# Kernel optimization log

Measured on AMD Instinct MI355X. Metric: run time of the kernel, lower is better.

## Reference

```python
import jax, jax.numpy as jnp
from jax import lax
import numpy as np

B, T, IN, H = 512, 2048, 6, 32


def _gru_dir(x, Wih, bih, Whh, bhh, reverse):
    # x: [B, T, in]; PyTorch GRU gate order: r, z, n
    xp = jnp.einsum('bti,gi->btg', x, Wih) + bih  # [B, T, 3H] precompute input GEMM
    h0 = jnp.zeros((x.shape[0], Whh.shape[1]), x.dtype)

    def step(h, xt):
        gh = h @ Whh.T + bhh                      # [B, 3H]
        xr, xz, xn = jnp.split(xt, 3, axis=-1)
        hr, hz, hn = jnp.split(gh, 3, axis=-1)
        r = jax.nn.sigmoid(xr + hr)
        z = jax.nn.sigmoid(xz + hz)
        n = jnp.tanh(xn + r * hn)
        h_new = (1.0 - z) * n + z * h
        return h_new, h_new

    xs = jnp.swapaxes(xp, 0, 1)                   # [T, B, 3H]
    _, hs = lax.scan(step, h0, xs, reverse=reverse)  # ys aligned to time index
    return jnp.swapaxes(hs, 0, 1)                 # [B, T, H]


def setup_inputs() -> dict:
    key = jax.random.key(0)
    ks = jax.random.split(key, 32)
    s = 1.0 / np.sqrt(H)
    u = lambda k, shp: jax.random.uniform(k, shp, jnp.float32, -s, s)
    inp = {'x': jax.random.normal(ks[0], (B, T, IN), jnp.float32)}
    i = 1
    for l, din in ((0, IN), (1, 2 * H)):
        for d in ('f', 'b'):
            inp[f'Wih_l{l}_{d}'] = u(ks[i], (3 * H, din)); i += 1
            inp[f'Whh_l{l}_{d}'] = u(ks[i], (3 * H, H)); i += 1
            inp[f'bih_l{l}_{d}'] = u(ks[i], (3 * H,)); i += 1
            inp[f'bhh_l{l}_{d}'] = u(ks[i], (3 * H,)); i += 1
    inp['fc1_w'] = u(ks[i], (16, 2 * H)); i += 1
    inp['fc1_b'] = u(ks[i], (16,)); i += 1
    inp['fc2_w'] = u(ks[i], (1, 16)); i += 1
    inp['fc2_b'] = u(ks[i], (1,))
    return inp


def reference(x, Wih_l0_f, Whh_l0_f, bih_l0_f, bhh_l0_f,
              Wih_l0_b, Whh_l0_b, bih_l0_b, bhh_l0_b,
              Wih_l1_f, Whh_l1_f, bih_l1_f, bhh_l1_f,
              Wih_l1_b, Whh_l1_b, bih_l1_b, bhh_l1_b,
              fc1_w, fc1_b, fc2_w, fc2_b):
    # layer 0 bidirectional
    f0 = _gru_dir(x, Wih_l0_f, bih_l0_f, Whh_l0_f, bhh_l0_f, reverse=False)
    b0 = _gru_dir(x, Wih_l0_b, bih_l0_b, Whh_l0_b, bhh_l0_b, reverse=True)
    h0 = jnp.concatenate([f0, b0], axis=-1)       # [B, T, 2H]; inter-layer dropout: eval mode -> identity
    # layer 1 bidirectional
    f1 = _gru_dir(h0, Wih_l1_f, bih_l1_f, Whh_l1_f, bhh_l1_f, reverse=False)
    b1 = _gru_dir(h0, Wih_l1_b, bih_l1_b, Whh_l1_b, bhh_l1_b, reverse=True)
    out = jnp.concatenate([f1, b1], axis=-1)      # [B, T, 2H]
    pooled = jnp.mean(out, axis=1)                # [B, 2H]
    h = jax.nn.relu(pooled @ fc1_w.T + fc1_b)     # dropout: eval mode -> identity
    return h @ fc2_w.T + fc2_b                    # [B, 1]
```

## Files before the change

kernel.cpp:

```cpp
#include <hip/hip_runtime.h>

#define TB  512
#define TT  2048
#define HID 32

typedef _Float16 f16;
typedef float f32x2 __attribute__((ext_vector_type(2)));


#define PKFMA(ACC, A, B) \
  asm("v_pk_fma_f32 %0, %1, %2, %0" : "+v"(ACC) : "v"(A), "v"(B))

#define TWO_LOG2E 2.88539008177792682f

__device__ __forceinline__ float half_swap(float x, int half){
#if __has_builtin(__builtin_amdgcn_permlane32_swap)
  typedef unsigned uv2 __attribute__((ext_vector_type(2)));
  uv2 r = __builtin_amdgcn_permlane32_swap(__float_as_uint(x), __float_as_uint(x),
                                           false, false);
  return __uint_as_float(half ? r.x : r.y);
#else
  (void)half;
  return __shfl_xor(x, 32, 64);
#endif
}

__global__ __launch_bounds__(64,1)
void gru_l0(const float* __restrict__ x,
            const float* __restrict__ Wih_f, const float* __restrict__ Whh_f,
            const float* __restrict__ bih_f, const float* __restrict__ bhh_f,
            const float* __restrict__ Wih_b, const float* __restrict__ Whh_b,
            const float* __restrict__ bih_b, const float* __restrict__ bhh_b,
            f16* __restrict__ h0)
{
  const int job  = blockIdx.x;
  const int b    = job >> 1;
  const int dir  = job & 1;
  const int lane = threadIdx.x;
  const int j    = lane & 31;
  const int half = lane >> 5;

  const float* Wih = dir ? Wih_b : Wih_f;
  const float* Whh = dir ? Whh_b : Whh_f;
  const float* bih = dir ? bih_b : bih_f;
  const float* bhh = dir ? bhh_b : bhh_f;

  const int mrow = half * 32 + j;
  const int nrow = 64 + j;

  f32x2 wh_m2[16], wh_n2[16];
  f32x2 wi_m2[3],  wi_n2[3];
  {
    const float4* wm4 = (const float4*)(Whh + mrow*32);
#pragma unroll
    for (int q=0;q<8;q++){ float4 v=wm4[q];
      wh_m2[2*q]   = f32x2{v.x, v.y};
      wh_m2[2*q+1] = f32x2{v.z, v.w}; }
    const float4* wn4 = (const float4*)(Whh + nrow*32);
#pragma unroll
    for (int q=0;q<8;q++){ float4 v=wn4[q];
      wh_n2[2*q]   = f32x2{v.x, v.y};
      wh_n2[2*q+1] = f32x2{v.z, v.w}; }
#pragma unroll
    for (int i=0;i<3;i++){
      wi_m2[i] = f32x2{Wih[mrow*6+2*i], Wih[mrow*6+2*i+1]};
      wi_n2[i] = f32x2{Wih[nrow*6+2*i], Wih[nrow*6+2*i+1]};
    }
  }
  const float b_m   = bih[mrow] + bhh[mrow];
  const float b_ihn = bih[nrow];
  const float b_hhn = bhh[nrow];

  __shared__ __align__(16) float hlds[32];

  double hj = 0.;
  float  hjf = 0.f;

  const long t0    = dir ? (TT-1) : 0;
  const long tstep = dir ? -1 : 1;
  const float* xrow = x + ((size_t)b*TT + t0)*6;
  const long  xinc = tstep*6;
  f16* hout = h0 + ((size_t)b*TT + t0)*64 + dir*32;
  const long hinc = tstep*64;

  f32x2 hp[16];
#pragma unroll
  for (int k=0;k<16;k++) hp[k]=f32x2{0.f,0.f};

#define L0_STEP(XV)                                                          \
  {                                                                          \
    f32x2 SX2 = f32x2{0.f,0.f}, SN2 = f32x2{0.f,0.f};                        \
    PKFMA(SX2, wi_m2[0], XV[0]); PKFMA(SN2, wi_n2[0], XV[0]);                \
    PKFMA(SX2, wi_m2[1], XV[1]); PKFMA(SN2, wi_n2[1], XV[1]);                \
    PKFMA(SX2, wi_m2[2], XV[2]); PKFMA(SN2, wi_n2[2], XV[2]);                \
    float sx  = SX2.x + SX2.y;                                               \
    float sxn = SN2.x + SN2.y;                                               \
    f32x2 A0=f32x2{0.f,0.f}, A1=f32x2{0.f,0.f};                              \
    f32x2 A2=f32x2{0.f,0.f}, A3=f32x2{0.f,0.f};                              \
    f32x2 C0=f32x2{0.f,0.f}, C1=f32x2{0.f,0.f};                              \
    f32x2 C2=f32x2{0.f,0.f}, C3=f32x2{0.f,0.f};                              \
    _Pragma("unroll")                                                        \
    for (int k=0;k<4;k++){                                                   \
      PKFMA(A0, wh_m2[4*k],   hp[4*k]);                                      \
      PKFMA(A1, wh_m2[4*k+1], hp[4*k+1]);                                    \
      PKFMA(A2, wh_m2[4*k+2], hp[4*k+2]);                                    \
      PKFMA(A3, wh_m2[4*k+3], hp[4*k+3]);                                    \
      PKFMA(C0, wh_n2[4*k],   hp[4*k]);                                      \
      PKFMA(C1, wh_n2[4*k+1], hp[4*k+1]);                                    \
      PKFMA(C2, wh_n2[4*k+2], hp[4*k+2]);                                    \
      PKFMA(C3, wh_n2[4*k+3], hp[4*k+3]);                                    \
    }                                                                        \
    f32x2 At = A0+A1+A2+A3;                                                  \
    f32x2 Ct = C0+C1+C2+C3;                                                  \
    float hm   = At.x + At.y;                                                \
    float sn_h = Ct.x + Ct.y;                                                \
    float vf   = hm + sx + b_m;                                              \
    float varg = half ? -vf : vf;                                            \
    float ef   = __builtin_amdgcn_exp2f(varg * -1.44269504088896341f);       \
    float gmf  = __builtin_amdgcn_rcpf(1.f + ef);                            \
    float wf   = half_swap(gmf, half);                                       \
    float c1 = (sxn + b_ihn) * TWO_LOG2E;                                    \
    float c2 = (sn_h + b_hhn) * TWO_LOG2E;                                   \
    float e2 = __builtin_amdgcn_exp2f(fmaf(gmf, c2, c1));                    \
    float nnf= 1.f - 2.f*__builtin_amdgcn_rcpf(1.f + e2);                    \
    float hnf = fmaf(wf, nnf - hjf, hjf);                                    \
    if (lane < 32){ hlds[j] = hnf; hout[j] = (f16)hnf; }                     \
    hout += hinc;                                                            \
    hj = fma((double)wf, (double)nnf - hj, hj);                              \
    hjf = (float)hj;                                                         \
    {                                                                        \
      const float4* h4 = (const float4*)hlds;                                \
      _Pragma("unroll")                                                      \
      for (int q=0;q<8;q++){ float4 v=h4[q];                                 \
        hp[2*q]   = f32x2{v.x, v.y};                                         \
        hp[2*q+1] = f32x2{v.z, v.w}; }                                       \
    }                                                                        \
  }

  f32x2 xa[3], xb[3];
  {
    const float2* p=(const float2*)xrow;
    xa[0]=f32x2{p[0].x,p[0].y}; xa[1]=f32x2{p[1].x,p[1].y}; xa[2]=f32x2{p[2].x,p[2].y};
    const float2* q=(const float2*)(xrow + xinc);
    xb[0]=f32x2{q[0].x,q[0].y}; xb[1]=f32x2{q[1].x,q[1].y}; xb[2]=f32x2{q[2].x,q[2].y};
  }
  const float* xld = xrow + 2*xinc;

#pragma unroll 1
  for (int it=0; it<TT; it+=2){
    L0_STEP(xa)
    if (it+2 < TT){
      const float2* p=(const float2*)xld;
      xa[0]=f32x2{p[0].x,p[0].y}; xa[1]=f32x2{p[1].x,p[1].y}; xa[2]=f32x2{p[2].x,p[2].y};
      xld += xinc;
    }
    L0_STEP(xb)
    if (it+3 < TT){
      const float2* p=(const float2*)xld;
      xb[0]=f32x2{p[0].x,p[0].y}; xb[1]=f32x2{p[1].x,p[1].y}; xb[2]=f32x2{p[2].x,p[2].y};
      xld += xinc;
    }
  }
#undef L0_STEP
}

__global__ __launch_bounds__(128,2)
void gru_l1(const f16* __restrict__ h0,
            const float* __restrict__ Wih_f, const float* __restrict__ Whh_f,
            const float* __restrict__ bih_f, const float* __restrict__ bhh_f,
            const float* __restrict__ Wih_b, const float* __restrict__ Whh_b,
            const float* __restrict__ bih_b, const float* __restrict__ bhh_b,
            float* __restrict__ pooled)
{
  const int job  = blockIdx.x;
  const int b    = job >> 1;
  const int dir  = job & 1;
  const int tid  = threadIdx.x;
  const int wid  = tid >> 6;
  const int lane = tid & 63;
  const int j    = lane & 31;
  const int half = lane >> 5;

  const float* Wih = dir ? Wih_b : Wih_f;
  const float* Whh = dir ? Whh_b : Whh_f;
  const float* bih = dir ? bih_b : bih_f;
  const float* bhh = dir ? bhh_b : bhh_f;

  const int mrow = half * 32 + j;
  const int nrow = 64 + j;

  __shared__ __align__(16) float hlds[32];
  __shared__ __align__(16) float ring[16*64];
  __shared__ __align__(16) float fx[16][64];
  __shared__ __align__(16) float fn[16][64];

  const f16* h0b = h0 + (size_t)b*TT*64;
#define ROWF(LT) (h0b + (size_t)(dir ? (TT-1-(LT)) : (LT))*64)

  f32x2 wreg[48];
  float b_m=0.f, b_ihn=0.f, b_hhn=0.f;

  if (wid == 1){
    const float4* wr4 = (const float4*)(Wih + (size_t)j*64      + half*32);
    const float4* wz4 = (const float4*)(Wih + (size_t)(32+j)*64 + half*32);
    const float4* wn4 = (const float4*)(Wih + (size_t)(64+j)*64 + half*32);
#pragma unroll
    for (int q=0;q<8;q++){ float4 v=wr4[q];
      wreg[2*q]   = f32x2{v.x,v.y};
      wreg[2*q+1] = f32x2{v.z,v.w}; }
#pragma unroll
    for (int q=0;q<8;q++){ float4 v=wz4[q];
      wreg[16+2*q]   = f32x2{v.x,v.y};
      wreg[16+2*q+1] = f32x2{v.z,v.w}; }
#pragma unroll
    for (int q=0;q<8;q++){ float4 v=wn4[q];
      wreg[32+2*q]   = f32x2{v.x,v.y};
      wreg[32+2*q+1] = f32x2{v.z,v.w}; }
  } else {
    const float4* hm4 = (const float4*)(Whh + mrow*32);
#pragma unroll
    for (int q=0;q<8;q++){ float4 v=hm4[q];
      wreg[2*q]   = f32x2{v.x,v.y};
      wreg[2*q+1] = f32x2{v.z,v.w}; }
    const float4* hn4 = (const float4*)(Whh + nrow*32);
#pragma unroll
    for (int q=0;q<8;q++){ float4 v=hn4[q];
      wreg[16+2*q]   = f32x2{v.x,v.y};
      wreg[16+2*q+1] = f32x2{v.z,v.w}; }
    b_m   = bih[mrow] + bhh[mrow];
    b_ihn = bih[nrow];
    b_hhn = bhh[nrow];
    if (lane < 32) hlds[lane] = 0.f;
  }

#define PRODUCE(S)                                                           \
  {                                                                          \
    const int slot = (S)&15;                                                 \
    const float4* s4 = (const float4*)(ring + slot*64 + half*32);            \
    f32x2 R0=f32x2{0.f,0.f}, R1=f32x2{0.f,0.f};                              \
    f32x2 Z0=f32x2{0.f,0.f}, Z1=f32x2{0.f,0.f};                              \
    f32x2 N0=f32x2{0.f,0.f}, N1=f32x2{0.f,0.f};                              \
    _Pragma("unroll")                                                        \
    for (int q=0;q<8;q++){ float4 v=s4[q];                                   \
      f32x2 lo = f32x2{v.x,v.y}, hi = f32x2{v.z,v.w};                        \
      PKFMA(R0, wreg[2*q],      lo);                                         \
      PKFMA(R1, wreg[2*q+1],    hi);                                         \
      PKFMA(Z0, wreg[16+2*q],   lo);                                         \
      PKFMA(Z1, wreg[16+2*q+1], hi);                                         \
      PKFMA(N0, wreg[32+2*q],   lo);                                         \
      PKFMA(N1, wreg[32+2*q+1], hi);                                         \
    }                                                                        \
    f32x2 Rt = R0+R1; f32x2 Zt = Z0+Z1; f32x2 Nt = N0+N1;                    \
    float rP = Rt.x+Rt.y, zP = Zt.x+Zt.y, nP = Nt.x+Nt.y;                    \
    float rF = rP + half_swap(rP, half);                                     \
    float zF = zP + half_swap(zP, half);                                     \
    fx[slot][lane] = half ? zF : rF;                                         \
    fn[slot][lane] = nP + half_swap(nP, half);                               \
  }

#define CORE(SX, SN)                                                         \
  {                                                                          \
    f32x2 A0=f32x2{0.f,0.f}, A1=f32x2{0.f,0.f};                              \
    f32x2 A2=f32x2{0.f,0.f}, A3=f32x2{0.f,0.f};                              \
    f32x2 C0=f32x2{0.f,0.f}, C1=f32x2{0.f,0.f};                              \
    f32x2 C2=f32x2{0.f,0.f}, C3=f32x2{0.f,0.f};                              \
    {                                                                        \
      const float4* h4 = (const float4*)hlds;                                \
      _Pragma("unroll")                                                      \
      for (int q=0;q<4;q++){                                                 \
        float4 v0=h4[2*q], v1=h4[2*q+1];                                     \
        f32x2 l0 = f32x2{v0.x,v0.y}, h0_ = f32x2{v0.z,v0.w};                 \
        f32x2 l1 = f32x2{v1.x,v1.y}, h1_ = f32x2{v1.z,v1.w};                 \
        PKFMA(A0, wreg[4*q],      l0);                                       \
        PKFMA(A1, wreg[4*q+1],    h0_);                                      \
        PKFMA(A2, wreg[4*q+2],    l1);                                       \
        PKFMA(A3, wreg[4*q+3],    h1_);                                      \
        PKFMA(C0, wreg[16+4*q],   l0);                                       \
        PKFMA(C1, wreg[16+4*q+1], h0_);                                      \
        PKFMA(C2, wreg[16+4*q+2], l1);                                       \
        PKFMA(C3, wreg[16+4*q+3], h1_);                                      \
      }                                                                      \
    }                                                                        \
    f32x2 At = A0+A1+A2+A3;                                                  \
    f32x2 Ct = C0+C1+C2+C3;                                                  \
    float hm   = At.x + At.y;                                                \
    float sn_h = Ct.x + Ct.y;                                                \
    float vf   = hm + (SX) + b_m;                                            \
    float varg = half ? -vf : vf;                                            \
    float ef   = __builtin_amdgcn_exp2f(varg * -1.44269504088896341f);       \
    float gmf  = __builtin_amdgcn_rcpf(1.f + ef);                            \
    float wf   = half_swap(gmf, half);                                       \
    float c1 = ((SN) + b_ihn) * TWO_LOG2E;                                   \
    float c2 = (sn_h + b_hhn) * TWO_LOG2E;                                   \
    float e2 = __builtin_amdgcn_exp2f(fmaf(gmf, c2, c1));                    \
    float nnf= 1.f - 2.f*__builtin_amdgcn_rcpf(1.f + e2);                    \
    float hnf = fmaf(wf, nnf - hjf, hjf);                                    \
    if (lane < 32) hlds[j] = hnf;                                            \
    hj = fma((double)wf, (double)nnf - hj, hj);                              \
    hjf = (float)hj;                                                         \
    psum += hj;                                                              \
  }

  double hj = 0., psum = 0.;
  float  hjf = 0.f;
  float pr[8];

  if (wid == 1){
    float pr0[16];
#pragma unroll
    for (int k=0;k<16;k++){
      int lt = k; if (lt > TT-1) lt = TT-1;
      pr0[k] = (float)ROWF(lt)[lane];
    }
#pragma unroll
    for (int k=0;k<16;k++) ring[k*64 + lane] = pr0[k];
#pragma unroll
    for (int k=0;k<8;k++){
      int lt = 16+k; if (lt > TT-1) lt = TT-1;
      pr[k] = (float)ROWF(lt)[lane];
    }
    PRODUCE(0) PRODUCE(1) PRODUCE(2) PRODUCE(3)
    PRODUCE(4) PRODUCE(5) PRODUCE(6) PRODUCE(7)
  }

#pragma unroll 1
  for (int t=0; t<TT; t+=8){
    __syncthreads();
    if (wid == 0){
      float sxa[8], sna[8];
#pragma unroll
      for (int k=0;k<8;k++){
        sxa[k] = fx[(t+k)&15][lane];
        sna[k] = fn[(t+k)&15][lane];
      }
      CORE(sxa[0], sna[0]) CORE(sxa[1], sna[1])
      CORE(sxa[2], sna[2]) CORE(sxa[3], sna[3])
      CORE(sxa[4], sna[4]) CORE(sxa[5], sna[5])
      CORE(sxa[6], sna[6]) CORE(sxa[7], sna[7])
    } else {
#pragma unroll
      for (int k=0;k<8;k++) ring[((t+16+k)&15)*64 + lane] = pr[k];
#pragma unroll
      for (int k=0;k<8;k++){
        int lt = t+24+k; if (lt > TT-1) lt = TT-1;
        pr[k] = (float)ROWF(lt)[lane];
      }
      if (t+8 <= TT-1){
        PRODUCE(t+8)
        PRODUCE(t+9) PRODUCE(t+10) PRODUCE(t+11)
        PRODUCE(t+12) PRODUCE(t+13) PRODUCE(t+14) PRODUCE(t+15)
      }
    }
  }
#undef PRODUCE
#undef CORE
#undef ROWF

  if (wid == 0 && lane < 32)
    pooled[(size_t)b*64 + dir*32 + j] = (float)psum;
}

__global__ void fc_ep(const float* __restrict__ pooled,
                      const float* __restrict__ fc1w, const float* __restrict__ fc1b,
                      const float* __restrict__ fc2w, const float* __restrict__ fc2b,
                      float* __restrict__ out)
{
  int b = blockIdx.x*blockDim.x + threadIdx.x;
  if (b >= TB) return;
  float v[64];
  const float4* p4 = (const float4*)(pooled + (size_t)b*64);
#pragma unroll
  for (int q=0;q<16;q++){ float4 t=p4[q];
    v[4*q]  =t.x*(1.f/TT); v[4*q+1]=t.y*(1.f/TT);
    v[4*q+2]=t.z*(1.f/TT); v[4*q+3]=t.w*(1.f/TT); }
  float acc = fc2b[0];
#pragma unroll
  for (int g=0; g<16; g++){
    float s = fc1b[g];
    const float4* w4 = (const float4*)(fc1w + g*64);
#pragma unroll
    for (int q=0;q<16;q++){ float4 w=w4[q];
      s=fmaf(w.x,v[4*q],s);   s=fmaf(w.y,v[4*q+1],s);
      s=fmaf(w.z,v[4*q+2],s); s=fmaf(w.w,v[4*q+3],s); }
    s = fmaxf(s, 0.f);
    acc = fmaf(fc2w[g], s, acc);
  }
  out[b] = acc;
}

extern "C" void kernel_launch(void* const* d_in, const int* in_sizes, int n_in,
                              void* d_out, int out_size, void* d_ws, size_t ws_size,
                              hipStream_t stream)
{
  (void)in_sizes; (void)n_in; (void)out_size;

  const float* x     = (const float*)d_in[0];
  const float* Wih0f = (const float*)d_in[1];
  const float* Whh0f = (const float*)d_in[2];
  const float* bih0f = (const float*)d_in[3];
  const float* bhh0f = (const float*)d_in[4];
  const float* Wih0b = (const float*)d_in[5];
  const float* Whh0b = (const float*)d_in[6];
  const float* bih0b = (const float*)d_in[7];
  const float* bhh0b = (const float*)d_in[8];
  const float* Wih1f = (const float*)d_in[9];
  const float* Whh1f = (const float*)d_in[10];
  const float* bih1f = (const float*)d_in[11];
  const float* bhh1f = (const float*)d_in[12];
  const float* Wih1b = (const float*)d_in[13];
  const float* Whh1b = (const float*)d_in[14];
  const float* bih1b = (const float*)d_in[15];
  const float* bhh1b = (const float*)d_in[16];
  const float* fc1w  = (const float*)d_in[17];
  const float* fc1b  = (const float*)d_in[18];
  const float* fc2w  = (const float*)d_in[19];
  const float* fc2b  = (const float*)d_in[20];

  const size_t POOLED_BYTES = (size_t)TB * 64 * sizeof(float);
  const size_t PER_B        = (size_t)TT * 64 * sizeof(f16);
  float* pooled = (float*)d_ws;
  f16*   h0     = (f16*)((char*)d_ws + POOLED_BYTES);

  size_t avail = (ws_size > POOLED_BYTES) ? (ws_size - POOLED_BYTES) : 0;
  int Bc = (int)(avail / PER_B);
  if (Bc < 1)  Bc = 1;
  if (Bc > TB) Bc = TB;
  int nch = (TB + Bc - 1) / Bc;
  int Bce = (TB + nch - 1) / nch;

  for (int b0 = 0; b0 < TB; b0 += Bce) {
    int bc = (TB - b0 < Bce) ? (TB - b0) : Bce;
    hipLaunchKernelGGL(gru_l0, dim3(2*bc), dim3(64), 0, stream,
                       x + (size_t)b0*TT*6,
                       Wih0f,Whh0f,bih0f,bhh0f, Wih0b,Whh0b,bih0b,bhh0b, h0);
    hipLaunchKernelGGL(gru_l1, dim3(2*bc), dim3(128), 0, stream,
                       h0,
                       Wih1f,Whh1f,bih1f,bhh1f, Wih1b,Whh1b,bih1b,bhh1b,
                       pooled + (size_t)b0*64);
  }
  hipLaunchKernelGGL(fc_ep, dim3(2), dim3(256), 0, stream,
                     pooled, fc1w, fc1b, fc2w, fc2b, (float*)d_out);
}
```

Before: 1.765 ms.

## Split recurrent matvec over K halves with cross-half reduction in both GRU layers

Previously each lane owned one full 32-long row: lanes 0-31 computed the r gate, lanes 32-63 the z gate, and every lane also computed the n row, so the n matvec was duplicated across halves. Now each half of the wave computes partial dot products over 16 of the 32 hidden inputs for all three gates, and the halves are combined with a permlane32 swap. This cuts per-lane FMAs on the serial critical path from 32 to 24 packed ops and halves the LDS reads of h per step. In exchange it adds three cross-half swaps per step, and every lane now evaluates both sigmoids redundantly.

```diff
diff --git a/kernel.cpp b/kernel.cpp
--- a/kernel.cpp
+++ b/kernel.cpp
@@ -11,6 +11,7 @@
 #define PKFMA(ACC, A, B) \
   asm("v_pk_fma_f32 %0, %1, %2, %0" : "+v"(ACC) : "v"(A), "v"(B))
 
+#define LOG2E     1.44269504088896341f
 #define TWO_LOG2E 2.88539008177792682f
 
 __device__ __forceinline__ float half_swap(float x, int half){
@@ -24,6 +25,19 @@
   return __shfl_xor(x, 32, 64);
 #endif
 }
+
+#define GATE_TAIL(HM_R, HM_Z, SN_H, XR, XZ, XNF)                             \
+    float vr = (HM_R) + (XR) + b_r;                                          \
+    float vz = (HM_Z) + (XZ) + b_z;                                          \
+    float er = __builtin_amdgcn_exp2f(vr * -LOG2E);                          \
+    float ez = __builtin_amdgcn_exp2f(vz *  LOG2E);                          \
+    float gr = __builtin_amdgcn_rcpf(1.f + er);                  \
+    float wf = __builtin_amdgcn_rcpf(1.f + ez);                 \
+    float c1 = ((XNF) + b_ihn) * TWO_LOG2E;                                  \
+    float c2 = ((SN_H) + b_hhn) * TWO_LOG2E;                                 \
+    float e2 = __builtin_amdgcn_exp2f(fmaf(gr, c2, c1));                     \
+    float nnf= 1.f - 2.f*__builtin_amdgcn_rcpf(1.f + e2);                    \
+    float hnf = fmaf(wf, nnf - hjf, hjf);
 
 __global__ __launch_bounds__(64,1)
 void gru_l0(const float* __restrict__ x,
@@ -45,31 +59,32 @@
   const float* bih = dir ? bih_b : bih_f;
   const float* bhh = dir ? bhh_b : bhh_f;
 
-  const int mrow = half * 32 + j;
-  const int nrow = 64 + j;
-
-  f32x2 wh_m2[16], wh_n2[16];
-  f32x2 wi_m2[3],  wi_n2[3];
+  f32x2 wr2[8], wz2[8], wn2[8];
+  f32x2 xwr[3], xwz[3], xwn[3];
   {
-    const float4* wm4 = (const float4*)(Whh + mrow*32);
-#pragma unroll
-    for (int q=0;q<8;q++){ float4 v=wm4[q];
-      wh_m2[2*q]   = f32x2{v.x, v.y};
-      wh_m2[2*q+1] = f32x2{v.z, v.w}; }
-    const float4* wn4 = (const float4*)(Whh + nrow*32);
-#pragma unroll
-    for (int q=0;q<8;q++){ float4 v=wn4[q];
-      wh_n2[2*q]   = f32x2{v.x, v.y};
-      wh_n2[2*q+1] = f32x2{v.z, v.w}; }
+    const float4* r4 = (const float4*)(Whh + (size_t)j*32      + half*16);
+    const float4* z4 = (const float4*)(Whh + (size_t)(32+j)*32 + half*16);
+    const float4* n4 = (const float4*)(Whh + (size_t)(64+j)*32 + half*16);
+#pragma unroll
+    for (int q=0;q<4;q++){ float4 v=r4[q];
+      wr2[2*q]=f32x2{v.x,v.y}; wr2[2*q+1]=f32x2{v.z,v.w}; }
+#pragma unroll
+    for (int q=0;q<4;q++){ float4 v=z4[q];
+      wz2[2*q]=f32x2{v.x,v.y}; wz2[2*q+1]=f32x2{v.z,v.w}; }
+#pragma unroll
+    for (int q=0;q<4;q++){ float4 v=n4[q];
+      wn2[2*q]=f32x2{v.x,v.y}; wn2[2*q+1]=f32x2{v.z,v.w}; }
 #pragma unroll
     for (int i=0;i<3;i++){
-      wi_m2[i] = f32x2{Wih[mrow*6+2*i], Wih[mrow*6+2*i+1]};
-      wi_n2[i] = f32x2{Wih[nrow*6+2*i], Wih[nrow*6+2*i+1]};
-    }
-  }
-  const float b_m   = bih[mrow] + bhh[mrow];
-  const float b_ihn = bih[nrow];
-  const float b_hhn = bhh[nrow];
+      xwr[i] = f32x2{Wih[(size_t)j*6+2*i],      Wih[(size_t)j*6+2*i+1]};
+      xwz[i] = f32x2{Wih[(size_t)(32+j)*6+2*i], Wih[(size_t)(32+j)*6+2*i+1]};
+      xwn[i] = f32x2{Wih[(size_t)(64+j)*6+2*i], Wih[(size_t)(64+j)*6+2*i+1]};
+    }
+  }
+  const float b_r   = bih[j]    + bhh[j];
+  const float b_z   = bih[32+j] + bhh[32+j];
+  const float b_ihn = bih[64+j];
+  const float b_hhn = bhh[64+j];
 
   __shared__ __align__(16) float hlds[32];
 
@@ -83,55 +98,43 @@
   f16* hout = h0 + ((size_t)b*TT + t0)*64 + dir*32;
   const long hinc = tstep*64;
 
-  f32x2 hp[16];
-#pragma unroll
-  for (int k=0;k<16;k++) hp[k]=f32x2{0.f,0.f};
+  f32x2 hp[8];
+#pragma unroll
+  for (int k=0;k<8;k++) hp[k]=f32x2{0.f,0.f};
 
 #define L0_STEP(XV)                                                          \
   {                                                                          \
-    f32x2 SX2 = f32x2{0.f,0.f}, SN2 = f32x2{0.f,0.f};                        \
-    PKFMA(SX2, wi_m2[0], XV[0]); PKFMA(SN2, wi_n2[0], XV[0]);                \
-    PKFMA(SX2, wi_m2[1], XV[1]); PKFMA(SN2, wi_n2[1], XV[1]);                \
-    PKFMA(SX2, wi_m2[2], XV[2]); PKFMA(SN2, wi_n2[2], XV[2]);                \
-    float sx  = SX2.x + SX2.y;                                               \
-    float sxn = SN2.x + SN2.y;                                               \
-    f32x2 A0=f32x2{0.f,0.f}, A1=f32x2{0.f,0.f};                              \
-    f32x2 A2=f32x2{0.f,0.f}, A3=f32x2{0.f,0.f};                              \
-    f32x2 C0=f32x2{0.f,0.f}, C1=f32x2{0.f,0.f};                              \
-    f32x2 C2=f32x2{0.f,0.f}, C3=f32x2{0.f,0.f};                              \
+    f32x2 XR2=f32x2{0.f,0.f}, XZ2=f32x2{0.f,0.f}, XN2=f32x2{0.f,0.f};        \
+    PKFMA(XR2, xwr[0], XV[0]); PKFMA(XZ2, xwz[0], XV[0]); PKFMA(XN2, xwn[0], XV[0]); \
+    PKFMA(XR2, xwr[1], XV[1]); PKFMA(XZ2, xwz[1], XV[1]); PKFMA(XN2, xwn[1], XV[1]); \
+    PKFMA(XR2, xwr[2], XV[2]); PKFMA(XZ2, xwz[2], XV[2]); PKFMA(XN2, xwn[2], XV[2]); \
+    float xr = XR2.x+XR2.y, xz = XZ2.x+XZ2.y, xnf = XN2.x+XN2.y;             \
+    f32x2 R0=f32x2{0.f,0.f}, R1=f32x2{0.f,0.f};                              \
+    f32x2 Z0=f32x2{0.f,0.f}, Z1=f32x2{0.f,0.f};                              \
+    f32x2 N0=f32x2{0.f,0.f}, N1=f32x2{0.f,0.f};                              \
     _Pragma("unroll")                                                        \
     for (int k=0;k<4;k++){                                                   \
-      PKFMA(A0, wh_m2[4*k],   hp[4*k]);                                      \
-      PKFMA(A1, wh_m2[4*k+1], hp[4*k+1]);                                    \
-      PKFMA(A2, wh_m2[4*k+2], hp[4*k+2]);                                    \
-      PKFMA(A3, wh_m2[4*k+3], hp[4*k+3]);                                    \
-      PKFMA(C0, wh_n2[4*k],   hp[4*k]);                                      \
-      PKFMA(C1, wh_n2[4*k+1], hp[4*k+1]);                                    \
-      PKFMA(C2, wh_n2[4*k+2], hp[4*k+2]);                                    \
-      PKFMA(C3, wh_n2[4*k+3], hp[4*k+3]);                                    \
+      PKFMA(R0, wr2[2*k],   hp[2*k]);                                        \
+      PKFMA(R1, wr2[2*k+1], hp[2*k+1]);                                      \
+      PKFMA(Z0, wz2[2*k],   hp[2*k]);                                        \
+      PKFMA(Z1, wz2[2*k+1], hp[2*k+1]);                                      \
+      PKFMA(N0, wn2[2*k],   hp[2*k]);                                        \
+      PKFMA(N1, wn2[2*k+1], hp[2*k+1]);                                      \
     }                                                                        \
-    f32x2 At = A0+A1+A2+A3;                                                  \
-    f32x2 Ct = C0+C1+C2+C3;                                                  \
-    float hm   = At.x + At.y;                                                \
-    float sn_h = Ct.x + Ct.y;                                                \
-    float vf   = hm + sx + b_m;                                              \
-    float varg = half ? -vf : vf;                                            \
-    float ef   = __builtin_amdgcn_exp2f(varg * -1.44269504088896341f);       \
-    float gmf  = __builtin_amdgcn_rcpf(1.f + ef);                            \
-    float wf   = half_swap(gmf, half);                                       \
-    float c1 = (sxn + b_ihn) * TWO_LOG2E;                                    \
-    float c2 = (sn_h + b_hhn) * TWO_LOG2E;                                   \
-    float e2 = __builtin_amdgcn_exp2f(fmaf(gmf, c2, c1));                    \
-    float nnf= 1.f - 2.f*__builtin_amdgcn_rcpf(1.f + e2);                    \
-    float hnf = fmaf(wf, nnf - hjf, hjf);                                    \
+    f32x2 Rt=R0+R1; f32x2 Zt=Z0+Z1; f32x2 Nt=N0+N1;                          \
+    float rP = Rt.x+Rt.y, zP = Zt.x+Zt.y, nP = Nt.x+Nt.y;                    \
+    float hm_r = rP + half_swap(rP, half);                                   \
+    float hm_z = zP + half_swap(zP, half);                                   \
+    float sn_h = nP + half_swap(nP, half);                                   \
+    GATE_TAIL(hm_r, hm_z, sn_h, xr, xz, xnf)                                 \
     if (lane < 32){ hlds[j] = hnf; hout[j] = (f16)hnf; }                     \
     hout += hinc;                                                            \
     hj = fma((double)wf, (double)nnf - hj, hj);                              \
     hjf = (float)hj;                                                         \
     {                                                                        \
-      const float4* h4 = (const float4*)hlds;                                \
+      const float4* h4 = (const float4*)(hlds + half*16);                    \
       _Pragma("unroll")                                                      \
-      for (int q=0;q<8;q++){ float4 v=h4[q];                                 \
+      for (int q=0;q<4;q++){ float4 v=h4[q];                                 \
         hp[2*q]   = f32x2{v.x, v.y};                                         \
         hp[2*q+1] = f32x2{v.z, v.w}; }                                       \
     }                                                                        \
@@ -186,19 +189,16 @@
   const float* bih = dir ? bih_b : bih_f;
   const float* bhh = dir ? bhh_b : bhh_f;
 
-  const int mrow = half * 32 + j;
-  const int nrow = 64 + j;
-
-  __shared__ __align__(16) float hlds[32];
-  __shared__ __align__(16) float ring[16*64];
-  __shared__ __align__(16) float fx[16][64];
-  __shared__ __align__(16) float fn[16][64];
+  __shared__ __align__(16) float  hlds[32];
+  __shared__ __align__(16) float  ring[16*64];
+  __shared__ __align__(16) float2 fxz[16][64];
+  __shared__ __align__(16) float  fnn[16][64];
 
   const f16* h0b = h0 + (size_t)b*TT*64;
 #define ROWF(LT) (h0b + (size_t)(dir ? (TT-1-(LT)) : (LT))*64)
 
   f32x2 wreg[48];
-  float b_m=0.f, b_ihn=0.f, b_hhn=0.f;
+  float b_r=0.f, b_z=0.f, b_ihn=0.f, b_hhn=0.f;
 
   if (wid == 1){
     const float4* wr4 = (const float4*)(Wih + (size_t)j*64      + half*32);
@@ -217,19 +217,22 @@
       wreg[32+2*q]   = f32x2{v.x,v.y};
       wreg[32+2*q+1] = f32x2{v.z,v.w}; }
   } else {
-    const float4* hm4 = (const float4*)(Whh + mrow*32);
-#pragma unroll
-    for (int q=0;q<8;q++){ float4 v=hm4[q];
-      wreg[2*q]   = f32x2{v.x,v.y};
-      wreg[2*q+1] = f32x2{v.z,v.w}; }
-    const float4* hn4 = (const float4*)(Whh + nrow*32);
-#pragma unroll
-    for (int q=0;q<8;q++){ float4 v=hn4[q];
-      wreg[16+2*q]   = f32x2{v.x,v.y};
-      wreg[16+2*q+1] = f32x2{v.z,v.w}; }
-    b_m   = bih[mrow] + bhh[mrow];
-    b_ihn = bih[nrow];
-    b_hhn = bhh[nrow];
+    const float4* r4 = (const float4*)(Whh + (size_t)j*32      + half*16);
+    const float4* z4 = (const float4*)(Whh + (size_t)(32+j)*32 + half*16);
+    const float4* n4 = (const float4*)(Whh + (size_t)(64+j)*32 + half*16);
+#pragma unroll
+    for (int q=0;q<4;q++){ float4 v=r4[q];
+      wreg[2*q]=f32x2{v.x,v.y}; wreg[2*q+1]=f32x2{v.z,v.w}; }
+#pragma unroll
+    for (int q=0;q<4;q++){ float4 v=z4[q];
+      wreg[8+2*q]=f32x2{v.x,v.y}; wreg[8+2*q+1]=f32x2{v.z,v.w}; }
+#pragma unroll
+    for (int q=0;q<4;q++){ float4 v=n4[q];
+      wreg[16+2*q]=f32x2{v.x,v.y}; wreg[16+2*q+1]=f32x2{v.z,v.w}; }
+    b_r   = bih[j]    + bhh[j];
+    b_z   = bih[32+j] + bhh[32+j];
+    b_ihn = bih[64+j];
+    b_hhn = bhh[64+j];
     if (lane < 32) hlds[lane] = 0.f;
   }
 
@@ -254,47 +257,34 @@
     float rP = Rt.x+Rt.y, zP = Zt.x+Zt.y, nP = Nt.x+Nt.y;                    \
     float rF = rP + half_swap(rP, half);                                     \
     float zF = zP + half_swap(zP, half);                                     \
-    fx[slot][lane] = half ? zF : rF;                                         \
-    fn[slot][lane] = nP + half_swap(nP, half);                               \
-  }
-
-#define CORE(SX, SN)                                                         \
+    fxz[slot][lane] = float2{rF, zF};                                        \
+    fnn[slot][lane] = nP + half_swap(nP, half);                              \
+  }
+
+#define CORE(FXZ, FN)                                                        \
   {                                                                          \
-    f32x2 A0=f32x2{0.f,0.f}, A1=f32x2{0.f,0.f};                              \
-    f32x2 A2=f32x2{0.f,0.f}, A3=f32x2{0.f,0.f};                              \
-    f32x2 C0=f32x2{0.f,0.f}, C1=f32x2{0.f,0.f};                              \
-    f32x2 C2=f32x2{0.f,0.f}, C3=f32x2{0.f,0.f};                              \
+    f32x2 R0=f32x2{0.f,0.f}, R1=f32x2{0.f,0.f};                              \
+    f32x2 Z0=f32x2{0.f,0.f}, Z1=f32x2{0.f,0.f};                              \
+    f32x2 N0=f32x2{0.f,0.f}, N1=f32x2{0.f,0.f};                              \
     {                                                                        \
-      const float4* h4 = (const float4*)hlds;                                \
+      const float4* h4 = (const float4*)(hlds + half*16);                    \
       _Pragma("unroll")                                                      \
-      for (int q=0;q<4;q++){                                                 \
-        float4 v0=h4[2*q], v1=h4[2*q+1];                                     \
-        f32x2 l0 = f32x2{v0.x,v0.y}, h0_ = f32x2{v0.z,v0.w};                 \
-        f32x2 l1 = f32x2{v1.x,v1.y}, h1_ = f32x2{v1.z,v1.w};                 \
-        PKFMA(A0, wreg[4*q],      l0);                                       \
-        PKFMA(A1, wreg[4*q+1],    h0_);                                      \
-        PKFMA(A2, wreg[4*q+2],    l1);                                       \
-        PKFMA(A3, wreg[4*q+3],    h1_);                                      \
-        PKFMA(C0, wreg[16+4*q],   l0);                                       \
-        PKFMA(C1, wreg[16+4*q+1], h0_);                                      \
-        PKFMA(C2, wreg[16+4*q+2], l1);                                       \
-        PKFMA(C3, wreg[16+4*q+3], h1_);                                      \
+      for (int q=0;q<4;q++){ float4 v=h4[q];                                 \
+        f32x2 lo = f32x2{v.x,v.y}, hi = f32x2{v.z,v.w};                      \
+        PKFMA(R0, wreg[2*q],      lo);                                       \
+        PKFMA(R1, wreg[2*q+1],    hi);                                       \
+        PKFMA(Z0, wreg[8+2*q],    lo);                                       \
+        PKFMA(Z1, wreg[8+2*q+1],  hi);                                       \
+        PKFMA(N0, wreg[16+2*q],   lo);                                       \
+        PKFMA(N1, wreg[16+2*q+1], hi);                                       \
       }                                                                      \
     }                                                                        \
-    f32x2 At = A0+A1+A2+A3;                                                  \
-    f32x2 Ct = C0+C1+C2+C3;                                                  \
-    float hm   = At.x + At.y;                                                \
-    float sn_h = Ct.x + Ct.y;                                                \
-    float vf   = hm + (SX) + b_m;                                            \
-    float varg = half ? -vf : vf;                                            \
-    float ef   = __builtin_amdgcn_exp2f(varg * -1.44269504088896341f);       \
-    float gmf  = __builtin_amdgcn_rcpf(1.f + ef);                            \
-    float wf   = half_swap(gmf, half);                                       \
-    float c1 = ((SN) + b_ihn) * TWO_LOG2E;                                   \
-    float c2 = (sn_h + b_hhn) * TWO_LOG2E;                                   \
-    float e2 = __builtin_amdgcn_exp2f(fmaf(gmf, c2, c1));                    \
-    float nnf= 1.f - 2.f*__builtin_amdgcn_rcpf(1.f + e2);                    \
-    float hnf = fmaf(wf, nnf - hjf, hjf);                                    \
+    f32x2 Rt=R0+R1; f32x2 Zt=Z0+Z1; f32x2 Nt=N0+N1;                          \
+    float rP = Rt.x+Rt.y, zP = Zt.x+Zt.y, nP = Nt.x+Nt.y;                    \
+    float hm_r = rP + half_swap(rP, half);                                   \
+    float hm_z = zP + half_swap(zP, half);                                   \
+    float sn_h = nP + half_swap(nP, half);                                   \
+    GATE_TAIL(hm_r, hm_z, sn_h, (FXZ).x, (FXZ).y, FN)                        \
     if (lane < 32) hlds[j] = hnf;                                            \
     hj = fma((double)wf, (double)nnf - hj, hj);                              \
     hjf = (float)hj;                                                         \
@@ -327,16 +317,16 @@
   for (int t=0; t<TT; t+=8){
     __syncthreads();
     if (wid == 0){
-      float sxa[8], sna[8];
+      float2 xz[8]; float fn[8];
 #pragma unroll
       for (int k=0;k<8;k++){
-        sxa[k] = fx[(t+k)&15][lane];
-        sna[k] = fn[(t+k)&15][lane];
+        xz[k] = fxz[(t+k)&15][lane];
+        fn[k] = fnn[(t+k)&15][lane];
       }
-      CORE(sxa[0], sna[0]) CORE(sxa[1], sna[1])
-      CORE(sxa[2], sna[2]) CORE(sxa[3], sna[3])
-      CORE(sxa[4], sna[4]) CORE(sxa[5], sna[5])
-      CORE(sxa[6], sna[6]) CORE(sxa[7], sna[7])
+      CORE(xz[0], fn[0]) CORE(xz[1], fn[1])
+      CORE(xz[2], fn[2]) CORE(xz[3], fn[3])
+      CORE(xz[4], fn[4]) CORE(xz[5], fn[5])
+      CORE(xz[6], fn[6]) CORE(xz[7], fn[7])
     } else {
 #pragma unroll
       for (int k=0;k<8;k++) ring[((t+16+k)&15)*64 + lane] = pr[k];
```

Measured after the change: 1.854 ms. 1.05x slower.
